# Kernel tuning notes

Measured on AMD Instinct MI355X. Metric: run time of the kernel, lower is better.

## Reference

```python
import jax, jax.numpy as jnp
import numpy as np

B = 8388608  # 2^23 samples
C = 2        # module's aux-mask construction hardcodes 2 label columns
ALPHA = 1.0


def setup_inputs() -> dict:
    key = jax.random.key(0)
    k1, k2 = jax.random.split(key)
    inputs = jax.random.normal(k1, (B, C), dtype=jnp.float32)
    # binary multi-label targets so that some rows are all-zero (mask matters)
    targets = (jax.random.uniform(k2, (B, C)) < 0.5).astype(jnp.float32)
    return {"inputs": inputs, "targets": targets}


def reference(inputs, targets):
    # BCE-with-logits, elementwise (reduce=False, pos_weight=None):
    #   loss = log(1 + exp(x)) - x * t  (numerically stable via logaddexp)
    bce = jnp.logaddexp(0.0, inputs) - inputs * targets
    # per-row mask: 1.0 if the row has any positive target, else 0.0
    # (original builds [B,2] with the same value in both columns -> broadcast [B,1])
    mask = (jnp.sum(targets, axis=1, keepdims=True) > 0).astype(bce.dtype)
    return jnp.mean(bce * mask * ALPHA)
```

## Files before the change

kernel.cpp:

```cpp
#include <hip/hip_runtime.h>
#include <hip/hip_bf16.h>

#define BLOCK 256
#define GRID  2048

__device__ __forceinline__ void bce4(const float4 xv, const float4 tv,
                                     float& sum_lin, float& prod) {
    const bool b0 = (tv.x + tv.y) > 0.0f;
    const bool b1 = (tv.z + tv.w) > 0.0f;
    const float m0 = b0 ? 1.0f : 0.0f;
    const float m1 = b1 ? 1.0f : 0.0f;

    const float f0 = 1.0f + __expf(-fabsf(xv.x));
    const float f1 = 1.0f + __expf(-fabsf(xv.y));
    const float f2 = 1.0f + __expf(-fabsf(xv.z));
    const float f3 = 1.0f + __expf(-fabsf(xv.w));
    prod *= b0 ? (f0 * f1) : 1.0f;
    prod *= b1 ? (f2 * f3) : 1.0f;

    const float r0 = __builtin_fmaf(-xv.x, tv.x, fmaxf(xv.x, 0.0f));
    const float r1 = __builtin_fmaf(-xv.y, tv.y, fmaxf(xv.y, 0.0f));
    const float r2 = __builtin_fmaf(-xv.z, tv.z, fmaxf(xv.z, 0.0f));
    const float r3 = __builtin_fmaf(-xv.w, tv.w, fmaxf(xv.w, 0.0f));
    sum_lin = __builtin_fmaf(m0, r0 + r1, sum_lin);
    sum_lin = __builtin_fmaf(m1, r2 + r3, sum_lin);
}

__global__ __launch_bounds__(BLOCK) void bce_partial_kernel(
        const float4* __restrict__ x4,
        const float4* __restrict__ t4,
        float* __restrict__ partials,
        int n4) {
    float sum_lin = 0.0f;
    float prod    = 1.0f;
    const int stride = gridDim.x * blockDim.x;
    for (int i = blockIdx.x * blockDim.x + threadIdx.x; i < n4; i += 2 * stride) {
        const float4 xa = x4[i];
        const float4 ta = t4[i];
        bce4(xa, ta, sum_lin, prod);
        const int j = i + stride;
        if (j < n4) {
            const float4 xb = x4[j];
            const float4 tb = t4[j];
            bce4(xb, tb, sum_lin, prod);
        }
    }
    float sum = sum_lin + __logf(prod);

    #pragma unroll
    for (int off = 32; off > 0; off >>= 1)
        sum += __shfl_down(sum, off, 64);

    __shared__ float wsum[BLOCK / 64];
    const int lane = threadIdx.x & 63;
    const int wid  = threadIdx.x >> 6;
    if (lane == 0) wsum[wid] = sum;
    __syncthreads();

    if (threadIdx.x == 0) {
        float b = 0.0f;
        #pragma unroll
        for (int w = 0; w < BLOCK / 64; ++w) b += wsum[w];
        partials[blockIdx.x] = b;
    }
}

__global__ __launch_bounds__(BLOCK) void bce_finalize_kernel(
        const float* __restrict__ partials,
        float* __restrict__ out,
        double inv_n) {
    double s = 0.0;
    #pragma unroll
    for (int k = 0; k < GRID / BLOCK; ++k)
        s += (double)partials[threadIdx.x + k * BLOCK];

    #pragma unroll
    for (int off = 32; off > 0; off >>= 1)
        s += __shfl_down(s, off, 64);

    __shared__ double wsum[BLOCK / 64];
    const int lane = threadIdx.x & 63;
    const int wid  = threadIdx.x >> 6;
    if (lane == 0) wsum[wid] = s;
    __syncthreads();

    if (threadIdx.x == 0) {
        double b = 0.0;
        #pragma unroll
        for (int w = 0; w < BLOCK / 64; ++w) b += wsum[w];
        out[0] = (float)(b * inv_n);
    }
}

extern "C" void kernel_launch(void* const* d_in, const int* in_sizes, int n_in,
                              void* d_out, int out_size, void* d_ws, size_t ws_size,
                              hipStream_t stream) {
    const float* x = (const float*)d_in[0];
    const float* t = (const float*)d_in[1];
    float* out = (float*)d_out;
    float* partials = (float*)d_ws;

    const int n  = in_sizes[0];
    const int n4 = n / 4;

    bce_partial_kernel<<<GRID, BLOCK, 0, stream>>>(
        (const float4*)x, (const float4*)t, partials, n4);

    bce_finalize_kernel<<<1, BLOCK, 0, stream>>>(partials, out, 1.0 / (double)n);
}
```

Baseline: 28.10 us.

## Fuse finalize into partial kernel via last-block atomic counter and fixed-size unrolled loads

Replaces the two-kernel reduction with a single kernel in which each block writes its partial, bumps an atomic counter, and the last block to arrive reduces all partials and writes the mean. For the known problem size, each thread also issues all of its float4 loads up front in a fully unrolled loop instead of a strided loop. This removes a second kernel launch and its dependency gap, and increases memory-level parallelism. The counter is never reset; the modulo check relies on it wrapping cleanly per call, and the workspace is assumed to start zeroed.

```diff
diff --git a/kernel.cpp b/kernel.cpp
--- a/kernel.cpp
+++ b/kernel.cpp
@@ -3,6 +3,8 @@
 
 #define BLOCK 256
 #define GRID  2048
+#define N_ELEM 16777216
+#define PT_V4 (N_ELEM / 4 / (GRID * BLOCK))
 
 __device__ __forceinline__ void bce4(const float4 xv, const float4 tv,
                                      float& sum_lin, float& prod) {
@@ -26,25 +28,24 @@
     sum_lin = __builtin_fmaf(m1, r2 + r3, sum_lin);
 }
 
-__global__ __launch_bounds__(BLOCK) void bce_partial_kernel(
+__global__ __launch_bounds__(BLOCK) void bce_fused_kernel(
         const float4* __restrict__ x4,
         const float4* __restrict__ t4,
         float* __restrict__ partials,
-        int n4) {
-    float sum_lin = 0.0f;
-    float prod    = 1.0f;
-    const int stride = gridDim.x * blockDim.x;
-    for (int i = blockIdx.x * blockDim.x + threadIdx.x; i < n4; i += 2 * stride) {
-        const float4 xa = x4[i];
-        const float4 ta = t4[i];
-        bce4(xa, ta, sum_lin, prod);
-        const int j = i + stride;
-        if (j < n4) {
-            const float4 xb = x4[j];
-            const float4 tb = t4[j];
-            bce4(xb, tb, sum_lin, prod);
-        }
-    }
+        unsigned int* __restrict__ counter,
+        float* __restrict__ out) {
+    const int tid    = blockIdx.x * BLOCK + threadIdx.x;
+    const int stride = GRID * BLOCK;
+
+    float4 xv[PT_V4], tv[PT_V4];
+    #pragma unroll
+    for (int k = 0; k < PT_V4; ++k) xv[k] = x4[tid + k * stride];
+    #pragma unroll
+    for (int k = 0; k < PT_V4; ++k) tv[k] = t4[tid + k * stride];
+
+    float sum_lin = 0.0f, prod = 1.0f;
+    #pragma unroll
+    for (int k = 0; k < PT_V4; ++k) bce4(xv[k], tv[k], sum_lin, prod);
     float sum = sum_lin + __logf(prod);
 
     #pragma unroll
@@ -52,44 +53,76 @@
         sum += __shfl_down(sum, off, 64);
 
     __shared__ float wsum[BLOCK / 64];
+    __shared__ bool  last_block;
     const int lane = threadIdx.x & 63;
     const int wid  = threadIdx.x >> 6;
     if (lane == 0) wsum[wid] = sum;
     __syncthreads();
 
     if (threadIdx.x == 0) {
-        float b = 0.0f;
+        float b = wsum[0] + wsum[1] + wsum[2] + wsum[3];
+        partials[blockIdx.x] = b;
+        __threadfence();
+        const unsigned int old = atomicAdd(counter, 1u);
+        last_block = ((old & (GRID - 1)) == (GRID - 1));
+    }
+    __syncthreads();
+
+    if (last_block) {
+        __threadfence();
+        volatile const float* vp = partials;
+        double s = 0.0;
         #pragma unroll
-        for (int w = 0; w < BLOCK / 64; ++w) b += wsum[w];
-        partials[blockIdx.x] = b;
+        for (int k = 0; k < GRID / BLOCK; ++k)
+            s += (double)vp[threadIdx.x + k * BLOCK];
+
+        #pragma unroll
+        for (int off = 32; off > 0; off >>= 1)
+            s += __shfl_down(s, off, 64);
+
+        __shared__ double dsum[BLOCK / 64];
+        if (lane == 0) dsum[wid] = s;
+        __syncthreads();
+        if (threadIdx.x == 0) {
+            const double b = dsum[0] + dsum[1] + dsum[2] + dsum[3];
+            out[0] = (float)(b * (1.0 / (double)N_ELEM));
+        }
     }
 }
 
-__global__ __launch_bounds__(BLOCK) void bce_finalize_kernel(
-        const float* __restrict__ partials,
-        float* __restrict__ out,
-        double inv_n) {
+__global__ __launch_bounds__(BLOCK) void bce_partial_generic(
+        const float4* __restrict__ x4, const float4* __restrict__ t4,
+        float* __restrict__ partials, int n4) {
+    float sum_lin = 0.0f, prod = 1.0f;
+    const int stride = gridDim.x * blockDim.x;
+    for (int i = blockIdx.x * blockDim.x + threadIdx.x; i < n4; i += stride) {
+        bce4(x4[i], t4[i], sum_lin, prod);
+    }
+    float sum = sum_lin + __logf(prod);
+    #pragma unroll
+    for (int off = 32; off > 0; off >>= 1) sum += __shfl_down(sum, off, 64);
+    __shared__ float wsum[BLOCK / 64];
+    const int lane = threadIdx.x & 63, wid = threadIdx.x >> 6;
+    if (lane == 0) wsum[wid] = sum;
+    __syncthreads();
+    if (threadIdx.x == 0)
+        partials[blockIdx.x] = wsum[0] + wsum[1] + wsum[2] + wsum[3];
+}
+
+__global__ __launch_bounds__(BLOCK) void bce_finalize_generic(
+        const float* __restrict__ partials, float* __restrict__ out, double inv_n) {
     double s = 0.0;
     #pragma unroll
     for (int k = 0; k < GRID / BLOCK; ++k)
         s += (double)partials[threadIdx.x + k * BLOCK];
-
     #pragma unroll
-    for (int off = 32; off > 0; off >>= 1)
-        s += __shfl_down(s, off, 64);
-
-    __shared__ double wsum[BLOCK / 64];
-    const int lane = threadIdx.x & 63;
-    const int wid  = threadIdx.x >> 6;
-    if (lane == 0) wsum[wid] = s;
+    for (int off = 32; off > 0; off >>= 1) s += __shfl_down(s, off, 64);
+    __shared__ double dsum[BLOCK / 64];
+    const int lane = threadIdx.x & 63, wid = threadIdx.x >> 6;
+    if (lane == 0) dsum[wid] = s;
     __syncthreads();
-
-    if (threadIdx.x == 0) {
-        double b = 0.0;
-        #pragma unroll
-        for (int w = 0; w < BLOCK / 64; ++w) b += wsum[w];
-        out[0] = (float)(b * inv_n);
-    }
+    if (threadIdx.x == 0)
+        out[0] = (float)((dsum[0] + dsum[1] + dsum[2] + dsum[3]) * inv_n);
 }
 
 extern "C" void kernel_launch(void* const* d_in, const int* in_sizes, int n_in,
@@ -99,12 +132,17 @@
     const float* t = (const float*)d_in[1];
     float* out = (float*)d_out;
     float* partials = (float*)d_ws;
+    unsigned int* counter = (unsigned int*)((char*)d_ws + GRID * sizeof(float));
 
-    const int n  = in_sizes[0];
-    const int n4 = n / 4;
+    const int n = in_sizes[0];
 
-    bce_partial_kernel<<<GRID, BLOCK, 0, stream>>>(
-        (const float4*)x, (const float4*)t, partials, n4);
-
-    bce_finalize_kernel<<<1, BLOCK, 0, stream>>>(partials, out, 1.0 / (double)n);
+    if (n == N_ELEM) {
+        bce_fused_kernel<<<GRID, BLOCK, 0, stream>>>(
+            (const float4*)x, (const float4*)t, partials, counter, out);
+    } else {
+        const int n4 = n / 4;
+        bce_partial_generic<<<GRID, BLOCK, 0, stream>>>(
+            (const float4*)x, (const float4*)t, partials, n4);
+        bce_finalize_generic<<<1, BLOCK, 0, stream>>>(partials, out, 1.0 / (double)n);
+    }
 }
```

Result: slower. 88.78 us (+216.0%).
